# Performance work log

Hardware: AMD Instinct MI355X
Metric: run time of the kernel (lower is better)

## Reference

```python
import jax
import jax.numpy as jnp
import numpy as np
from jax import lax

TAU = 1.0
EPS = 1e-20


def setup_inputs() -> dict:
    key = jax.random.key(0)
    ks = jax.random.split(key, 8)
    B, n, M, G = 256, 128, 512, 512  # batch, seq, mem_size, global dim
    SLOTS = 15                        # his_mem slots (mem_slots - 1)
    d_q = M + G
    his_mem = jax.random.normal(ks[0], (B, SLOTS, M), dtype=jnp.float32)
    states = jax.random.normal(ks[1], (B, n, M), dtype=jnp.float32)
    states_mask = jnp.round(jax.random.uniform(ks[2], (B, n), dtype=jnp.float32))
    global_trace = jax.random.normal(ks[3], (B, G), dtype=jnp.float32)
    null_mem = jnp.zeros((B, 1, M), dtype=jnp.float32)
    gumbel_u = jax.random.uniform(ks[4], (B, n, SLOTS + 1), dtype=jnp.float32)
    attn_W = jax.random.normal(ks[5], (M, d_q + M), dtype=jnp.float32) * 0.02
    attn_b = jax.random.normal(ks[6], (M,), dtype=jnp.float32) * 0.02
    stdv = 1.0 / np.sqrt(M)
    v = jax.random.normal(ks[7], (M,), dtype=jnp.float32) * stdv
    return {"his_mem": his_mem, "states": states, "states_mask": states_mask,
            "global_trace": global_trace, "null_mem": null_mem,
            "gumbel_u": gumbel_u, "attn_W": attn_W, "attn_b": attn_b, "v": v}


def _gumbel_softmax_hard(logits, u, tau):
    # deterministic gumbel noise from uniform samples u in [0,1)
    g = -jnp.log(-jnp.log(jnp.clip(u, EPS, 1.0)) + EPS)
    y_soft = jax.nn.softmax((logits + g) / tau, axis=-1)
    y_hard = jax.nn.one_hot(jnp.argmax(y_soft, axis=-1), logits.shape[-1],
                            dtype=y_soft.dtype)
    # straight-through estimator (matches torch F.gumbel_softmax hard=True)
    return y_hard - lax.stop_gradient(y_soft) + y_soft


def _forward(his_mem, states, states_mask, global_trace, null_mem,
             gumbel_u, attn_W, attn_b, v):
    B, n, M = states.shape
    S = his_mem.shape[1] + 1  # mem_slots (including null slot)

    def step(hm, xs):
        state, mask, u = xs  # [B,M], [B], [B,S]
        mem = jnp.concatenate([hm, null_mem], axis=1)          # [B,S,M]
        query = jnp.concatenate([state, global_trace], axis=1)  # [B,d_q]
        q = jnp.broadcast_to(query[:, None, :], (B, S, query.shape[-1]))
        energy = jnp.tanh(jnp.concatenate([q, mem], axis=2) @ attn_W.T + attn_b)
        attn_energies = energy @ v                              # [B,S]
        attn_weights = jax.nn.softmax(attn_energies, axis=-1)
        empty_mask = (jnp.sum(jnp.abs(mem), axis=-1) == 0).astype(attn_weights.dtype)
        attn_weights = attn_weights + empty_mask * 10.0
        slot_select = _gumbel_softmax_hard(attn_weights, u, TAU)  # [B,S]
        write_mask = (slot_select[:, : S - 1] * mask[:, None])[:, :, None]  # [B,S-1,1]
        hm = (1.0 - write_mask) * hm + write_mask * state[:, None, :]
        return hm, slot_select

    xs = (jnp.swapaxes(states, 0, 1),        # [n,B,M]
          jnp.swapaxes(states_mask, 0, 1),   # [n,B]
          jnp.swapaxes(gumbel_u, 0, 1))      # [n,B,S]
    hm_final, log = lax.scan(step, his_mem, xs)
    write_log = jnp.swapaxes(log, 0, 1)      # [B,n,S]
    return hm_final, write_log


def reference(his_mem, states, states_mask, global_trace, null_mem,
              gumbel_u, attn_W, attn_b, v):
    return _forward(his_mem, states, states_mask, global_trace, null_mem,
                    gumbel_u, attn_W, attn_b, v)
```

## Files before the change

### kernel.cpp

```cpp
#include <hip/hip_runtime.h>

constexpr int kB = 256;
constexpr int kN = 128;
constexpr int kM = 512;
constexpr int kSlots = 15;
constexpr int kS = 16;
constexpr int kW = 1536;
constexpr int kCap = 8192;

__device__ __forceinline__ float tanh_fast(float x)
{
    float xc = fminf(15.f, fmaxf(-15.f, x));
    float ex = __expf(2.f * xc);
    return 1.f - 2.f * __builtin_amdgcn_rcpf(ex + 1.f);
}

__global__ __launch_bounds__(256) void prep1_k(
    const float* __restrict__ his_mem, const float* __restrict__ null_mem,
    const float* __restrict__ gumbel_u, float* __restrict__ out,
    int* __restrict__ empty0, int* __restrict__ cnt, int* __restrict__ total,
    unsigned* __restrict__ list, int* __restrict__ listPos,
    int* __restrict__ ambBatch, unsigned char* __restrict__ amb_flags)
{
    const int b = blockIdx.x;
    const int tid = threadIdx.x;
    const int wave = tid >> 6, lane = tid & 63;
    __shared__ int eflag[kS];
    float* out_hm = out;
    float* out_log = out + (size_t)kB * kSlots * kM;

    for (int s = wave; s < kS; s += 4) {
        const float* p = (s < kSlots) ? his_mem + (size_t)(b * kSlots + s) * kM
                                      : null_mem + (size_t)b * kM;
        float4 v0 = *(const float4*)(p + lane * 4);
        float4 v1 = *(const float4*)(p + 256 + lane * 4);
        int nz = (v0.x != 0.f) | (v0.y != 0.f) | (v0.z != 0.f) | (v0.w != 0.f) |
                 (v1.x != 0.f) | (v1.y != 0.f) | (v1.z != 0.f) | (v1.w != 0.f);
        unsigned long long bal = __ballot(nz);
        if (lane == 0) eflag[s] = (bal == 0ull) ? 1 : 0;
        if (s < kSlots) {
            float* dst = out_hm + (size_t)(b * kSlots + s) * kM;
            *(float4*)(dst + lane * 4) = v0;
            *(float4*)(dst + 256 + lane * 4) = v1;
        }
    }
    __syncthreads();
    if (tid < kS) empty0[b * kS + tid] = eflag[tid];

    if (tid < kN) {
        const int idx = b * kN + tid;
        const float* up = gumbel_u + (size_t)idx * kS;
        float g[kS];
#pragma unroll
        for (int s = 0; s < kS; ++s) {
            float u = fminf(fmaxf(up[s], 1e-20f), 1.0f);
            g[s] = -logf(-logf(u) + 1e-20f);
        }
        float rhs = g[15] + 10.f * (eflag[15] ? 1.f : 0.f) - 1.01f;
        bool amb = false;
#pragma unroll
        for (int s = 0; s < kSlots; ++s)
            amb = amb || (g[s] + 10.f * (eflag[s] ? 1.f : 0.f) >= rhs);
        amb_flags[idx] = amb ? 1 : 0;
        if (amb) {
            int pos = atomicAdd(&total[0], 1);
            if (pos < kCap) list[pos] = (unsigned)idx;
            listPos[idx] = pos;
            int prev = atomicAdd(&cnt[b], 1);
            if (prev == 0) {
                int bp = atomicAdd(&total[1], 1);
                ambBatch[bp] = b;
            }
        }
        float* lp = out_log + (size_t)idx * kS;
        float4 zz = make_float4(0.f, 0.f, 0.f, 0.f);
        *(float4*)(lp + 0) = zz;
        *(float4*)(lp + 4) = zz;
        *(float4*)(lp + 8) = zz;
        *(float4*)(lp + 12) = make_float4(0.f, 0.f, 0.f, 1.f);
    }
}

__global__ __launch_bounds__(256) void prep2_k(
    const float* __restrict__ W, const float* __restrict__ his_mem,
    const float* __restrict__ null_mem, const float* __restrict__ states,
    const float* __restrict__ global_trace, const float* __restrict__ attn_b,
    const int* __restrict__ total, const int* __restrict__ ambBatch,
    const unsigned* __restrict__ list, float* __restrict__ C0,
    float* __restrict__ qCache, float* __restrict__ cwCache,
    int* __restrict__ stepNz)
{
    const int tid = threadIdx.x;

    if (blockIdx.x < 512) {
        const int nab = total[1];
        const int cx = blockIdx.x >> 3;
        const int cy = blockIdx.x & 7;
        if (cx * 4 >= nab) return;
        __shared__ float As[16 * 68];
        __shared__ float Bs[16 * 68];
        const int n0 = cy * 64;
        const int row_l = tid >> 2;
        const int k4 = (tid & 3) * 4;
        const int ty = tid >> 4, tx = tid & 15;

        int bi = cx * 4 + (row_l >> 4);
        if (bi >= nab) bi = nab - 1;
        const int b = ambBatch[bi];
        const int s = row_l & 15;
        const float* ap = (s < kSlots) ? (his_mem + (size_t)(b * kSlots + s) * kM)
                                       : (null_mem + (size_t)b * kM);
        const float* wp = W + (size_t)(n0 + row_l) * kW + 1024;

        float acc[4][4];
#pragma unroll
        for (int i = 0; i < 4; ++i)
#pragma unroll
            for (int j = 0; j < 4; ++j) acc[i][j] = 0.f;

        for (int kt = 0; kt < kM; kt += 16) {
            float4 a4 = *(const float4*)(ap + kt + k4);
            float4 b4 = *(const float4*)(wp + kt + k4);
            __syncthreads();
            As[(k4 + 0) * 68 + row_l] = a4.x; As[(k4 + 1) * 68 + row_l] = a4.y;
            As[(k4 + 2) * 68 + row_l] = a4.z; As[(k4 + 3) * 68 + row_l] = a4.w;
            Bs[(k4 + 0) * 68 + row_l] = b4.x; Bs[(k4 + 1) * 68 + row_l] = b4.y;
            Bs[(k4 + 2) * 68 + row_l] = b4.z; Bs[(k4 + 3) * 68 + row_l] = b4.w;
            __syncthreads();
#pragma unroll
            for (int k = 0; k < 16; ++k) {
                const float4 av = *(const float4*)&As[k * 68 + ty * 4];
                const float4 bv = *(const float4*)&Bs[k * 68 + tx * 4];
                acc[0][0] = fmaf(av.x, bv.x, acc[0][0]);
                acc[0][1] = fmaf(av.x, bv.y, acc[0][1]);
                acc[0][2] = fmaf(av.x, bv.z, acc[0][2]);
                acc[0][3] = fmaf(av.x, bv.w, acc[0][3]);
                acc[1][0] = fmaf(av.y, bv.x, acc[1][0]);
                acc[1][1] = fmaf(av.y, bv.y, acc[1][1]);
                acc[1][2] = fmaf(av.y, bv.z, acc[1][2]);
                acc[1][3] = fmaf(av.y, bv.w, acc[1][3]);
                acc[2][0] = fmaf(av.z, bv.x, acc[2][0]);
                acc[2][1] = fmaf(av.z, bv.y, acc[2][1]);
                acc[2][2] = fmaf(av.z, bv.z, acc[2][2]);
                acc[2][3] = fmaf(av.z, bv.w, acc[2][3]);
                acc[3][0] = fmaf(av.w, bv.x, acc[3][0]);
                acc[3][1] = fmaf(av.w, bv.y, acc[3][1]);
                acc[3][2] = fmaf(av.w, bv.z, acc[3][2]);
                acc[3][3] = fmaf(av.w, bv.w, acc[3][3]);
            }
        }
#pragma unroll
        for (int i = 0; i < 4; ++i) {
            int rl = ty * 4 + i;
            int bij = cx * 4 + (rl >> 4);
            if (bij >= nab) bij = nab - 1;
            int ro = ambBatch[bij] * kS + (rl & 15);
            float4 o = make_float4(acc[i][0], acc[i][1], acc[i][2], acc[i][3]);
            *(float4*)(C0 + (size_t)ro * kM + n0 + tx * 4) = o;
        }
    } else {
        int n = total[0];
        if (n > kCap) n = kCap;
        __shared__ float Xs[1024];
        __shared__ int nzs;

        for (int c = (int)blockIdx.x - 512; c < n * 16; c += 2048) {
            const int i = c >> 4;
            const int j = c & 15;
            const int idx = (int)list[i];
            const int b = idx >> 7;
            __syncthreads();
            if (tid == 0) nzs = 0;
            __syncthreads();
            float s0 = states[(size_t)idx * kM + tid];
            float s1 = states[(size_t)idx * kM + 256 + tid];
            Xs[tid] = s0; Xs[256 + tid] = s1;
            Xs[512 + tid] = global_trace[(size_t)b * kM + tid];
            Xs[768 + tid] = global_trace[(size_t)b * kM + 256 + tid];
            if (s0 != 0.f || s1 != 0.f) nzs = 1;
            __syncthreads();

            const int g = tid >> 4;
            const int l = tid & 15;
#pragma unroll
            for (int p = 0; p < 2; ++p) {
                const int r = j * 32 + p * 16 + g;
                const float* wr = W + (size_t)r * kW;
                float accq = 0.f, accc = 0.f;
#pragma unroll
                for (int jj = 0; jj < 16; ++jj) {
                    int k = l * 4 + jj * 64;
                    float4 w4 = *(const float4*)(wr + k);
                    float4 x4 = *(const float4*)&Xs[k];
                    accq = fmaf(w4.x, x4.x, accq); accq = fmaf(w4.y, x4.y, accq);
                    accq = fmaf(w4.z, x4.z, accq); accq = fmaf(w4.w, x4.w, accq);
                }
#pragma unroll
                for (int jj = 0; jj < 8; ++jj) {
                    int k = l * 4 + jj * 64;
                    float4 w4 = *(const float4*)(wr + 1024 + k);
                    float4 x4 = *(const float4*)&Xs[k];
                    accc = fmaf(w4.x, x4.x, accc); accc = fmaf(w4.y, x4.y, accc);
                    accc = fmaf(w4.z, x4.z, accc); accc = fmaf(w4.w, x4.w, accc);
                }
                accq += __shfl_xor(accq, 1); accq += __shfl_xor(accq, 2);
                accq += __shfl_xor(accq, 4); accq += __shfl_xor(accq, 8);
                accc += __shfl_xor(accc, 1); accc += __shfl_xor(accc, 2);
                accc += __shfl_xor(accc, 4); accc += __shfl_xor(accc, 8);
                if (l == 0) {
                    qCache[(size_t)i * kM + r] = accq + attn_b[r];
                    cwCache[(size_t)i * kM + r] = accc;
                }
            }
            if (tid == 0 && j == 0) stepNz[i] = nzs;
        }
    }
}

constexpr int kCsStride = 528;

__global__ __launch_bounds__(256) void phaseB_k(
    const float* __restrict__ C0, const int* __restrict__ empty0,
    const unsigned char* __restrict__ amb_flags, const int* __restrict__ cnt,
    const int* __restrict__ listPos, const float* __restrict__ qCache,
    const float* __restrict__ cwCache, const int* __restrict__ stepNz,
    const float* __restrict__ states, const float* __restrict__ states_mask,
    const float* __restrict__ gumbel_u, const float* __restrict__ global_trace,
    const float* __restrict__ W, const float* __restrict__ attn_b,
    const float* __restrict__ v, float* __restrict__ out)
{
    const int b = blockIdx.x;
    if (cnt[b] == 0) return;
    const int tid = threadIdx.x;
    float* out_hm = out;
    float* out_log = out + (size_t)kB * kSlots * kM;

    __shared__ float Cs[kS * kCsStride];
    __shared__ float Xb[1024];
    __shared__ float Qb[kM];
    __shared__ float vs[kM];
    __shared__ float e_sh[kS];
    __shared__ float empty_sh[kS];
    __shared__ unsigned char flS[kN];
    __shared__ int slot_src[kSlots];
    __shared__ int k_sh, wk_sh, nz_sh;

    for (int i = tid; i < kS * kM; i += 256) {
        int s = i >> 9, m = i & 511;
        Cs[s * kCsStride + m] = C0[(size_t)(b * kS + s) * kM + m];
    }
    for (int i = tid; i < kM; i += 256) {
        vs[i] = v[i];
        Xb[512 + i] = global_trace[(size_t)b * kM + i];
    }
    if (tid < kS) empty_sh[tid] = empty0[b * kS + tid] ? 1.0f : 0.0f;
    if (tid < kSlots) slot_src[tid] = -1;
    if (tid < kN) flS[tid] = amb_flags[b * kN + tid];
    __syncthreads();

    const int sidx = tid >> 4;
    const int ml = tid & 15;

    for (int t = 0; t < kN; ++t) {
        if (!flS[t]) continue;

        const int pos = listPos[b * kN + t];
        const float* qp;
        if (pos < kCap) {
            qp = qCache + (size_t)pos * kM;
        } else {
            Xb[tid] = states[(size_t)(b * kN + t) * kM + tid];
            Xb[256 + tid] = states[(size_t)(b * kN + t) * kM + 256 + tid];
            __syncthreads();
            const int g2 = tid >> 4, l2 = tid & 15;
            for (int r0 = 0; r0 < kM; r0 += 16) {
                int r = r0 + g2;
                const float* wr = W + (size_t)r * kW;
                float a = 0.f;
                for (int k = l2 * 4; k < 1024; k += 64) {
                    float4 w4 = *(const float4*)(wr + k);
                    float4 x4 = *(const float4*)&Xb[k];
                    a = fmaf(w4.x, x4.x, a); a = fmaf(w4.y, x4.y, a);
                    a = fmaf(w4.z, x4.z, a); a = fmaf(w4.w, x4.w, a);
                }
                a += __shfl_xor(a, 1); a += __shfl_xor(a, 2);
                a += __shfl_xor(a, 4); a += __shfl_xor(a, 8);
                if (l2 == 0) Qb[r] = a + attn_b[r];
            }
            __syncthreads();
            qp = Qb;
        }

        const float* crow = &Cs[sidx * kCsStride];
        float acc = 0.f;
#pragma unroll
        for (int j = 0; j < 8; ++j) {
            int m = ml * 4 + j * 64;
            float4 q4 = *(const float4*)(qp + m);
            float4 c4 = *(const float4*)&crow[m];
            float4 v4 = *(const float4*)&vs[m];
            acc = fmaf(v4.x, tanh_fast(q4.x + c4.x), acc);
            acc = fmaf(v4.y, tanh_fast(q4.y + c4.y), acc);
            acc = fmaf(v4.z, tanh_fast(q4.z + c4.z), acc);
            acc = fmaf(v4.w, tanh_fast(q4.w + c4.w), acc);
        }
        acc += __shfl_xor(acc, 1); acc += __shfl_xor(acc, 2);
        acc += __shfl_xor(acc, 4); acc += __shfl_xor(acc, 8);
        if (ml == 0) e_sh[sidx] = acc;
        __syncthreads();

        if (tid < 64) {
            int s = tid;
            float ev = (s < kS) ? e_sh[s] : -3.0e38f;
            float mx = ev;
            mx = fmaxf(mx, __shfl_xor(mx, 1));
            mx = fmaxf(mx, __shfl_xor(mx, 2));
            mx = fmaxf(mx, __shfl_xor(mx, 4));
            mx = fmaxf(mx, __shfl_xor(mx, 8));
            float w = (s < kS) ? __expf(ev - mx) : 0.f;
            float sm = w;
            sm += __shfl_xor(sm, 1); sm += __shfl_xor(sm, 2);
            sm += __shfl_xor(sm, 4); sm += __shfl_xor(sm, 8);
            w = w / sm;
            w += 10.0f * ((s < kS) ? empty_sh[s] : 0.f);
            float z;
            if (s < kS) {
                float u = gumbel_u[(size_t)(b * kN + t) * kS + s];
                u = fminf(fmaxf(u, 1e-20f), 1.0f);
                float g = -logf(-logf(u) + 1e-20f);
                z = w + g;
            } else z = -3.0e38f;
            float zm = z;
            zm = fmaxf(zm, __shfl_xor(zm, 1));
            zm = fmaxf(zm, __shfl_xor(zm, 2));
            zm = fmaxf(zm, __shfl_xor(zm, 4));
            zm = fmaxf(zm, __shfl_xor(zm, 8));
            unsigned long long bal = __ballot(z == zm) & 0xFFFFull;
            if (s == 0) k_sh = __ffsll(bal) - 1;
        }
        __syncthreads();

        const int k = k_sh;
        if (tid < kS) out_log[(size_t)(b * kN + t) * kS + tid] = (tid == k) ? 1.f : 0.f;
        if (tid == 0) {
            float mv = states_mask[b * kN + t];
            wk_sh = (k < kSlots && mv != 0.0f) ? k : -1;
            nz_sh = 0;
        }
        __syncthreads();

        const int wk = wk_sh;
        if (wk >= 0) {
            if (pos < kCap) {
                Cs[wk * kCsStride + tid] = cwCache[(size_t)pos * kM + tid];
                Cs[wk * kCsStride + 256 + tid] = cwCache[(size_t)pos * kM + 256 + tid];
                if (tid == 0) {
                    slot_src[wk] = t;
                    empty_sh[wk] = stepNz[pos] ? 0.f : 1.f;
                }
            } else {
                if (Xb[tid] != 0.f || Xb[256 + tid] != 0.f) nz_sh = 1;
                __syncthreads();
                const int g2 = tid >> 4, l2 = tid & 15;
                for (int r0 = 0; r0 < kM; r0 += 16) {
                    int r = r0 + g2;
                    const float* wr = W + (size_t)r * kW + 1024;
                    float ca = 0.f;
                    for (int k2 = l2 * 4; k2 < kM; k2 += 64) {
                        float4 w4 = *(const float4*)(wr + k2);
                        float4 x4 = *(const float4*)&Xb[k2];
                        ca = fmaf(w4.x, x4.x, ca); ca = fmaf(w4.y, x4.y, ca);
                        ca = fmaf(w4.z, x4.z, ca); ca = fmaf(w4.w, x4.w, ca);
                    }
                    ca += __shfl_xor(ca, 1); ca += __shfl_xor(ca, 2);
                    ca += __shfl_xor(ca, 4); ca += __shfl_xor(ca, 8);
                    if (l2 == 0) Cs[wk * kCsStride + r] = ca;
                }
                __syncthreads();
                if (tid == 0) {
                    slot_src[wk] = t;
                    empty_sh[wk] = nz_sh ? 0.f : 1.f;
                }
            }
        }
        __syncthreads();
    }

    for (int s = 0; s < kSlots; ++s) {
        int ts = slot_src[s];
        if (ts >= 0) {
            float* dst = out_hm + (size_t)(b * kSlots + s) * kM;
            dst[tid] = states[(size_t)(b * kN + ts) * kM + tid];
            dst[tid + 256] = states[(size_t)(b * kN + ts) * kM + tid + 256];
        }
    }
}

extern "C" void kernel_launch(void* const* d_in, const int* in_sizes, int n_in,
                              void* d_out, int out_size, void* d_ws, size_t ws_size,
                              hipStream_t stream)
{
    const float* his_mem      = (const float*)d_in[0];
    const float* states       = (const float*)d_in[1];
    const float* states_mask  = (const float*)d_in[2];
    const float* global_trace = (const float*)d_in[3];
    const float* null_mem     = (const float*)d_in[4];
    const float* gumbel_u     = (const float*)d_in[5];
    const float* attn_W       = (const float*)d_in[6];
    const float* attn_b       = (const float*)d_in[7];
    const float* v            = (const float*)d_in[8];

    float* C0 = (float*)d_ws;
    float* qCache = C0 + (size_t)kB * kS * kM;
    float* cwCache = qCache + (size_t)kCap * kM;
    int* cnt = (int*)(cwCache + (size_t)kCap * kM);
    int* total = cnt + kB;
    int* empty0 = total + 16;
    int* ambBatch = empty0 + kB * kS;
    int* stepNz = ambBatch + kB;
    int* listPos = stepNz + kCap;
    unsigned* list = (unsigned*)(listPos + kB * kN);
    unsigned char* amb = (unsigned char*)(list + kB * kN);

    hipMemsetAsync(cnt, 0, (kB + 16) * sizeof(int), stream);
    prep1_k<<<kB, 256, 0, stream>>>(his_mem, null_mem, gumbel_u, (float*)d_out,
                                    empty0, cnt, total, list, listPos, ambBatch,
                                    amb);
    prep2_k<<<2560, 256, 0, stream>>>(attn_W, his_mem, null_mem, states,
                                      global_trace, attn_b, total, ambBatch,
                                      list, C0, qCache, cwCache, stepNz);
    phaseB_k<<<kB, 256, 0, stream>>>(C0, empty0, amb, cnt, listPos, qCache,
                                     cwCache, stepNz, states, states_mask,
                                     gumbel_u, global_trace, attn_W, attn_b, v,
                                     (float*)d_out);
}
```

Baseline: 169.7 us.

## Replace global atomic ambiguity lists with per-batch fixed segments and per-batch GEMV

Drops the global atomic work list and the memset. prep1 now builds a per-batch list of up to 16 ambiguous steps using a wave ballot and prefix popcount. prep2 launches a fixed grid: per-batch blocks compute the memory-projection C0 as a shared-memory GEMV, and per-batch-segment blocks precompute query and write caches for the first 16 ambiguous steps. Batches with more than 16 ambiguous steps fall back to computing those steps inside phaseB, so the cost grows if ambiguity is dense.

New measurement: 196.8 us. 15.9% more time.

```diff
diff --git a/kernel.cpp b/kernel.cpp
--- a/kernel.cpp
+++ b/kernel.cpp
@@ -6,7 +6,7 @@
 constexpr int kSlots = 15;
 constexpr int kS = 16;
 constexpr int kW = 1536;
-constexpr int kCap = 8192;
+constexpr int kSeg = 16;
 
 __device__ __forceinline__ float tanh_fast(float x)
 {
@@ -18,14 +18,14 @@
 __global__ __launch_bounds__(256) void prep1_k(
     const float* __restrict__ his_mem, const float* __restrict__ null_mem,
     const float* __restrict__ gumbel_u, float* __restrict__ out,
-    int* __restrict__ empty0, int* __restrict__ cnt, int* __restrict__ total,
-    unsigned* __restrict__ list, int* __restrict__ listPos,
-    int* __restrict__ ambBatch, unsigned char* __restrict__ amb_flags)
+    int* __restrict__ empty0, int* __restrict__ cnt, int* __restrict__ ambList,
+    unsigned char* __restrict__ amb_flags)
 {
     const int b = blockIdx.x;
     const int tid = threadIdx.x;
     const int wave = tid >> 6, lane = tid & 63;
     __shared__ int eflag[kS];
+    __shared__ int wcnt[4];
     float* out_hm = out;
     float* out_log = out + (size_t)kB * kSlots * kM;
 
@@ -47,6 +47,7 @@
     __syncthreads();
     if (tid < kS) empty0[b * kS + tid] = eflag[tid];
 
+    bool amb = false;
     if (tid < kN) {
         const int idx = b * kN + tid;
         const float* up = gumbel_u + (size_t)idx * kS;
@@ -57,21 +58,10 @@
             g[s] = -logf(-logf(u) + 1e-20f);
         }
         float rhs = g[15] + 10.f * (eflag[15] ? 1.f : 0.f) - 1.01f;
-        bool amb = false;
 #pragma unroll
         for (int s = 0; s < kSlots; ++s)
             amb = amb || (g[s] + 10.f * (eflag[s] ? 1.f : 0.f) >= rhs);
         amb_flags[idx] = amb ? 1 : 0;
-        if (amb) {
-            int pos = atomicAdd(&total[0], 1);
-            if (pos < kCap) list[pos] = (unsigned)idx;
-            listPos[idx] = pos;
-            int prev = atomicAdd(&cnt[b], 1);
-            if (prev == 0) {
-                int bp = atomicAdd(&total[1], 1);
-                ambBatch[bp] = b;
-            }
-        }
         float* lp = out_log + (size_t)idx * kS;
         float4 zz = make_float4(0.f, 0.f, 0.f, 0.f);
         *(float4*)(lp + 0) = zz;
@@ -79,109 +69,97 @@
         *(float4*)(lp + 8) = zz;
         *(float4*)(lp + 12) = make_float4(0.f, 0.f, 0.f, 1.f);
     }
+    unsigned long long bal = __ballot(amb);
+    if (lane == 0) wcnt[wave] = __popcll(bal);
+    __syncthreads();
+    if (tid < kN && amb) {
+        int j = __popcll(bal & ((1ull << lane) - 1)) + (wave == 1 ? wcnt[0] : 0);
+        if (j < kSeg) ambList[b * kSeg + j] = tid;
+    }
+    if (tid == 0) cnt[b] = wcnt[0] + wcnt[1];
 }
 
 __global__ __launch_bounds__(256) void prep2_k(
     const float* __restrict__ W, const float* __restrict__ his_mem,
     const float* __restrict__ null_mem, const float* __restrict__ states,
     const float* __restrict__ global_trace, const float* __restrict__ attn_b,
-    const int* __restrict__ total, const int* __restrict__ ambBatch,
-    const unsigned* __restrict__ list, float* __restrict__ C0,
-    float* __restrict__ qCache, float* __restrict__ cwCache,
-    int* __restrict__ stepNz)
+    const int* __restrict__ cnt, const int* __restrict__ ambList,
+    float* __restrict__ C0, float* __restrict__ qCache,
+    float* __restrict__ cwCache, int* __restrict__ stepNz)
 {
     const int tid = threadIdx.x;
-
-    if (blockIdx.x < 512) {
-        const int nab = total[1];
-        const int cx = blockIdx.x >> 3;
-        const int cy = blockIdx.x & 7;
-        if (cx * 4 >= nab) return;
-        __shared__ float As[16 * 68];
-        __shared__ float Bs[16 * 68];
-        const int n0 = cy * 64;
-        const int row_l = tid >> 2;
-        const int k4 = (tid & 3) * 4;
-        const int ty = tid >> 4, tx = tid & 15;
-
-        int bi = cx * 4 + (row_l >> 4);
-        if (bi >= nab) bi = nab - 1;
-        const int b = ambBatch[bi];
-        const int s = row_l & 15;
-        const float* ap = (s < kSlots) ? (his_mem + (size_t)(b * kSlots + s) * kM)
-                                       : (null_mem + (size_t)b * kM);
-        const float* wp = W + (size_t)(n0 + row_l) * kW + 1024;
-
-        float acc[4][4];
-#pragma unroll
-        for (int i = 0; i < 4; ++i)
-#pragma unroll
-            for (int j = 0; j < 4; ++j) acc[i][j] = 0.f;
-
-        for (int kt = 0; kt < kM; kt += 16) {
-            float4 a4 = *(const float4*)(ap + kt + k4);
-            float4 b4 = *(const float4*)(wp + kt + k4);
-            __syncthreads();
-            As[(k4 + 0) * 68 + row_l] = a4.x; As[(k4 + 1) * 68 + row_l] = a4.y;
-            As[(k4 + 2) * 68 + row_l] = a4.z; As[(k4 + 3) * 68 + row_l] = a4.w;
-            Bs[(k4 + 0) * 68 + row_l] = b4.x; Bs[(k4 + 1) * 68 + row_l] = b4.y;
-            Bs[(k4 + 2) * 68 + row_l] = b4.z; Bs[(k4 + 3) * 68 + row_l] = b4.w;
-            __syncthreads();
-#pragma unroll
-            for (int k = 0; k < 16; ++k) {
-                const float4 av = *(const float4*)&As[k * 68 + ty * 4];
-                const float4 bv = *(const float4*)&Bs[k * 68 + tx * 4];
-                acc[0][0] = fmaf(av.x, bv.x, acc[0][0]);
-                acc[0][1] = fmaf(av.x, bv.y, acc[0][1]);
-                acc[0][2] = fmaf(av.x, bv.z, acc[0][2]);
-                acc[0][3] = fmaf(av.x, bv.w, acc[0][3]);
-                acc[1][0] = fmaf(av.y, bv.x, acc[1][0]);
-                acc[1][1] = fmaf(av.y, bv.y, acc[1][1]);
-                acc[1][2] = fmaf(av.y, bv.z, acc[1][2]);
-                acc[1][3] = fmaf(av.y, bv.w, acc[1][3]);
-                acc[2][0] = fmaf(av.z, bv.x, acc[2][0]);
-                acc[2][1] = fmaf(av.z, bv.y, acc[2][1]);
-                acc[2][2] = fmaf(av.z, bv.z, acc[2][2]);
-                acc[2][3] = fmaf(av.z, bv.w, acc[2][3]);
-                acc[3][0] = fmaf(av.w, bv.x, acc[3][0]);
-                acc[3][1] = fmaf(av.w, bv.y, acc[3][1]);
-                acc[3][2] = fmaf(av.w, bv.z, acc[3][2]);
-                acc[3][3] = fmaf(av.w, bv.w, acc[3][3]);
-            }
-        }
-#pragma unroll
-        for (int i = 0; i < 4; ++i) {
-            int rl = ty * 4 + i;
-            int bij = cx * 4 + (rl >> 4);
-            if (bij >= nab) bij = nab - 1;
-            int ro = ambBatch[bij] * kS + (rl & 15);
-            float4 o = make_float4(acc[i][0], acc[i][1], acc[i][2], acc[i][3]);
-            *(float4*)(C0 + (size_t)ro * kM + n0 + tx * 4) = o;
+    __shared__ float sbuf[kS * 520];
+    __shared__ int nzs;
+
+    if (blockIdx.x < 2048) {
+        const int b = blockIdx.x >> 3;
+        if (cnt[b] == 0) return;
+        const int n0 = (blockIdx.x & 7) * 64;
+        for (int i = tid; i < kS * (kM / 4); i += 256) {
+            int s = i >> 7;
+            int c4 = (i & 127) * 4;
+            const float* p = (s < kSlots) ? his_mem + (size_t)(b * kSlots + s) * kM
+                                          : null_mem + (size_t)b * kM;
+            *(float4*)&sbuf[s * 520 + c4] = *(const float4*)(p + c4);
+        }
+        __syncthreads();
+        const int g = tid >> 4, l = tid & 15;
+#pragma unroll
+        for (int cc = 0; cc < 4; ++cc) {
+            const int col = n0 + cc * 16 + g;
+            const float* wr = W + (size_t)col * kW + 1024;
+            float acc[kS];
+#pragma unroll
+            for (int s = 0; s < kS; ++s) acc[s] = 0.f;
+#pragma unroll 2
+            for (int jj = 0; jj < 8; ++jj) {
+                int k = l * 4 + jj * 64;
+                float4 w4 = *(const float4*)(wr + k);
+#pragma unroll
+                for (int s = 0; s < kS; ++s) {
+                    float4 m4 = *(const float4*)&sbuf[s * 520 + k];
+                    acc[s] = fmaf(w4.x, m4.x, acc[s]);
+                    acc[s] = fmaf(w4.y, m4.y, acc[s]);
+                    acc[s] = fmaf(w4.z, m4.z, acc[s]);
+                    acc[s] = fmaf(w4.w, m4.w, acc[s]);
+                }
+            }
+#pragma unroll
+            for (int s = 0; s < kS; ++s) {
+                acc[s] += __shfl_xor(acc[s], 1);
+                acc[s] += __shfl_xor(acc[s], 2);
+                acc[s] += __shfl_xor(acc[s], 4);
+                acc[s] += __shfl_xor(acc[s], 8);
+            }
+            if (l == 0) {
+#pragma unroll
+                for (int s = 0; s < kS; ++s)
+                    C0[(size_t)(b * kS + s) * kM + col] = acc[s];
+            }
         }
     } else {
-        int n = total[0];
-        if (n > kCap) n = kCap;
-        __shared__ float Xs[1024];
-        __shared__ int nzs;
-
-        for (int c = (int)blockIdx.x - 512; c < n * 16; c += 2048) {
-            const int i = c >> 4;
-            const int j = c & 15;
-            const int idx = (int)list[i];
-            const int b = idx >> 7;
+        const int u = (int)blockIdx.x - 2048;
+        const int b = u >> 4;
+        const int j = u & 15;
+        int nc = cnt[b];
+        if (nc == 0) return;
+        if (nc > kSeg) nc = kSeg;
+
+        for (int i = 0; i < nc; ++i) {
+            const int t = ambList[b * kSeg + i];
+            const int idx = b * kN + t;
             __syncthreads();
             if (tid == 0) nzs = 0;
             __syncthreads();
             float s0 = states[(size_t)idx * kM + tid];
             float s1 = states[(size_t)idx * kM + 256 + tid];
-            Xs[tid] = s0; Xs[256 + tid] = s1;
-            Xs[512 + tid] = global_trace[(size_t)b * kM + tid];
-            Xs[768 + tid] = global_trace[(size_t)b * kM + 256 + tid];
+            sbuf[tid] = s0; sbuf[256 + tid] = s1;
+            sbuf[512 + tid] = global_trace[(size_t)b * kM + tid];
+            sbuf[768 + tid] = global_trace[(size_t)b * kM + 256 + tid];
             if (s0 != 0.f || s1 != 0.f) nzs = 1;
             __syncthreads();
 
-            const int g = tid >> 4;
-            const int l = tid & 15;
+            const int g = tid >> 4, l = tid & 15;
 #pragma unroll
             for (int p = 0; p < 2; ++p) {
                 const int r = j * 32 + p * 16 + g;
@@ -191,7 +169,7 @@
                 for (int jj = 0; jj < 16; ++jj) {
                     int k = l * 4 + jj * 64;
                     float4 w4 = *(const float4*)(wr + k);
-                    float4 x4 = *(const float4*)&Xs[k];
+                    float4 x4 = *(const float4*)&sbuf[k];
                     accq = fmaf(w4.x, x4.x, accq); accq = fmaf(w4.y, x4.y, accq);
                     accq = fmaf(w4.z, x4.z, accq); accq = fmaf(w4.w, x4.w, accq);
                 }
@@ -199,7 +177,7 @@
                 for (int jj = 0; jj < 8; ++jj) {
                     int k = l * 4 + jj * 64;
                     float4 w4 = *(const float4*)(wr + 1024 + k);
-                    float4 x4 = *(const float4*)&Xs[k];
+                    float4 x4 = *(const float4*)&sbuf[k];
                     accc = fmaf(w4.x, x4.x, accc); accc = fmaf(w4.y, x4.y, accc);
                     accc = fmaf(w4.z, x4.z, accc); accc = fmaf(w4.w, x4.w, accc);
                 }
@@ -208,11 +186,11 @@
                 accc += __shfl_xor(accc, 1); accc += __shfl_xor(accc, 2);
                 accc += __shfl_xor(accc, 4); accc += __shfl_xor(accc, 8);
                 if (l == 0) {
-                    qCache[(size_t)i * kM + r] = accq + attn_b[r];
-                    cwCache[(size_t)i * kM + r] = accc;
-                }
-            }
-            if (tid == 0 && j == 0) stepNz[i] = nzs;
+                    qCache[(size_t)(b * kSeg + i) * kM + r] = accq + attn_b[r];
+                    cwCache[(size_t)(b * kSeg + i) * kM + r] = accc;
+                }
+            }
+            if (tid == 0 && j == 0) stepNz[b * kSeg + i] = nzs;
         }
     }
 }
@@ -222,12 +200,12 @@
 __global__ __launch_bounds__(256) void phaseB_k(
     const float* __restrict__ C0, const int* __restrict__ empty0,
     const unsigned char* __restrict__ amb_flags, const int* __restrict__ cnt,
-    const int* __restrict__ listPos, const float* __restrict__ qCache,
-    const float* __restrict__ cwCache, const int* __restrict__ stepNz,
-    const float* __restrict__ states, const float* __restrict__ states_mask,
-    const float* __restrict__ gumbel_u, const float* __restrict__ global_trace,
-    const float* __restrict__ W, const float* __restrict__ attn_b,
-    const float* __restrict__ v, float* __restrict__ out)
+    const float* __restrict__ qCache, const float* __restrict__ cwCache,
+    const int* __restrict__ stepNz, const float* __restrict__ states,
+    const float* __restrict__ states_mask, const float* __restrict__ gumbel_u,
+    const float* __restrict__ global_trace, const float* __restrict__ W,
+    const float* __restrict__ attn_b, const float* __restrict__ v,
+    float* __restrict__ out)
 {
     const int b = blockIdx.x;
     if (cnt[b] == 0) return;
@@ -261,12 +239,15 @@
     const int sidx = tid >> 4;
     const int ml = tid & 15;
 
+    int jloc = 0;
     for (int t = 0; t < kN; ++t) {
         if (!flS[t]) continue;
-
-        const int pos = listPos[b * kN + t];
+        const bool cached = (jloc < kSeg);
+        const int pos = b * kSeg + jloc;
+        ++jloc;
+
         const float* qp;
-        if (pos < kCap) {
+        if (cached) {
             qp = qCache + (size_t)pos * kM;
         } else {
             Xb[tid] = states[(size_t)(b * kN + t) * kM + tid];
@@ -351,7 +332,7 @@
 
         const int wk = wk_sh;
         if (wk >= 0) {
-            if (pos < kCap) {
+            if (cached) {
                 Cs[wk * kCsStride + tid] = cwCache[(size_t)pos * kM + tid];
                 Cs[wk * kCsStride + 256 + tid] = cwCache[(size_t)pos * kM + 256 + tid];
                 if (tid == 0) {
@@ -412,25 +393,20 @@
 
     float* C0 = (float*)d_ws;
     float* qCache = C0 + (size_t)kB * kS * kM;
-    float* cwCache = qCache + (size_t)kCap * kM;
-    int* cnt = (int*)(cwCache + (size_t)kCap * kM);
-    int* total = cnt + kB;
-    int* empty0 = total + 16;
-    int* ambBatch = empty0 + kB * kS;
-    int* stepNz = ambBatch + kB;
-    int* listPos = stepNz + kCap;
-    unsigned* list = (unsigned*)(listPos + kB * kN);
-    unsigned char* amb = (unsigned char*)(list + kB * kN);
-
-    hipMemsetAsync(cnt, 0, (kB + 16) * sizeof(int), stream);
+    float* cwCache = qCache + (size_t)kB * kSeg * kM;
+    int* empty0 = (int*)(cwCache + (size_t)kB * kSeg * kM);
+    int* cnt = empty0 + kB * kS;
+    int* ambList = cnt + kB;
+    int* stepNz = ambList + kB * kSeg;
+    unsigned char* amb = (unsigned char*)(stepNz + kB * kSeg);
+
     prep1_k<<<kB, 256, 0, stream>>>(his_mem, null_mem, gumbel_u, (float*)d_out,
-                                    empty0, cnt, total, list, listPos, ambBatch,
-                                    amb);
-    prep2_k<<<2560, 256, 0, stream>>>(attn_W, his_mem, null_mem, states,
-                                      global_trace, attn_b, total, ambBatch,
-                                      list, C0, qCache, cwCache, stepNz);
-    phaseB_k<<<kB, 256, 0, stream>>>(C0, empty0, amb, cnt, listPos, qCache,
-                                     cwCache, stepNz, states, states_mask,
-                                     gumbel_u, global_trace, attn_W, attn_b, v,
+                                    empty0, cnt, ambList, amb);
+    prep2_k<<<6144, 256, 0, stream>>>(attn_W, his_mem, null_mem, states,
+                                      global_trace, attn_b, cnt, ambList,
+                                      C0, qCache, cwCache, stepNz);
+    phaseB_k<<<kB, 256, 0, stream>>>(C0, empty0, amb, cnt, qCache, cwCache,
+                                     stepNz, states, states_mask, gumbel_u,
+                                     global_trace, attn_W, attn_b, v,
                                      (float*)d_out);
 }
```
